# Optimization experiments

Measured on AMD Instinct MI355X. Metric: run time of the kernel, lower is better.

Reference implementation:

```python
import jax, jax.numpy as jnp
import numpy as np

N, B, CIN = 2048, 16, 1
M = 4096
COUT = 64
R = 128


def setup_inputs() -> dict:
    key = jax.random.key(0)
    k1, k2, k3, k4, k5 = jax.random.split(key, 5)
    return {
        "context_in": jax.random.normal(k1, (N, B, CIN), dtype=jnp.float32),
        "context_out": jax.random.normal(k2, (N, B, COUT), dtype=jnp.float32),
        "target_in": jax.random.normal(k3, (M, B, CIN), dtype=jnp.float32),
        "lengthscale": jnp.ones((1,), dtype=jnp.float32),
        "W": jax.random.normal(k4, (R, COUT + 1), dtype=jnp.float32),
        "b": jax.random.normal(k5, (R,), dtype=jnp.float32),
    }


def reference(context_in, context_out, target_in, lengthscale, W, b):
    # context_in: (N,B,Cin), context_out: (N,B,Cout), target_in: (M,B,Cin)
    n, batch, _ = context_in.shape
    # density channel prepended -> (N,B,Cout+1)
    dens = jnp.ones((n, batch, 1), dtype=context_in.dtype)
    co = jnp.concatenate([dens, context_out], axis=-1)
    ci = jnp.transpose(context_in, (1, 0, 2))   # (B,N,Cin)
    ti = jnp.transpose(target_in, (1, 0, 2))    # (B,M,Cin)
    # squared pairwise distances (B,N,M)
    d2 = (jnp.sum(ci * ci, -1)[:, :, None]
          + jnp.sum(ti * ti, -1)[:, None, :]
          - 2.0 * jnp.einsum('bnd,bmd->bnm', ci, ti))
    d2 = jnp.maximum(d2, 0.0)
    # RBF kernel: exp(-0.5 * d2 / lengthscale^2)
    K = jnp.exp(-0.5 * d2 / (lengthscale[0] ** 2))  # (B,N,M)
    # weighted sum over context points: (B,M,Cout+1)
    out = jnp.einsum('nbc,bnm->bmc', co, K)
    # density normalization of non-density channels
    out = jnp.concatenate([out[..., :1], out[..., 1:] / (out[..., :1] + 1e-8)], axis=-1)
    # linear projection (Cout+1 -> R)
    out = out @ W.T + b
    return jnp.transpose(out, (1, 0, 2))  # (M,B,R)
```

## Files before the change

kernel.cpp:

```cpp
#include <hip/hip_runtime.h>
#include <hip/hip_bf16.h>


#define N_CTX 2048
#define BATCH 16
#define M_TGT 4096
#define COUT  64
#define RDIM  128

#define WS_CO_BYTES (N_CTX * BATCH * COUT * 2)
#define WS_SXA_OFF  WS_CO_BYTES
#define WS_SXB_OFF  (WS_SXA_OFF + N_CTX * BATCH * 4)
#define WS_WT_OFF   (WS_SXB_OFF + N_CTX * BATCH * 4)

#define SSCALE 0.8493222f

typedef __attribute__((ext_vector_type(8)))  short        bf16x8;
typedef __attribute__((ext_vector_type(4)))  float        floatx4;
typedef __attribute__((ext_vector_type(4)))  unsigned int uint4v;

#if __has_builtin(__builtin_amdgcn_exp2f)
#define EXP2F __builtin_amdgcn_exp2f
#else
#define EXP2F exp2f
#endif

static __device__ __forceinline__ unsigned int pack_bf16(float lo, float hi) {
    __hip_bfloat162 h = __float22bfloat162_rn(make_float2(lo, hi));
    return *reinterpret_cast<unsigned int*>(&h);
}
static __device__ __forceinline__ unsigned short f2bf(float f) {
    __hip_bfloat16 h = __float2bfloat16(f);
    return *reinterpret_cast<unsigned short*>(&h);
}

__global__ __launch_bounds__(256)
void convdeepset_prep(const float* __restrict__ ci, const float* __restrict__ co,
                      const float* __restrict__ ls, const float* __restrict__ W,
                      unsigned char* __restrict__ ws)
{
    unsigned short* cow = (unsigned short*)ws;
    float*          sxa = (float*)(ws + WS_SXA_OFF);
    float*          sxb = (float*)(ws + WS_SXB_OFF);
    unsigned short* wt  = (unsigned short*)(ws + WS_WT_OFF);
    const int blk = blockIdx.x, tid = threadIdx.x;

    if (blk < 1024) {
        const int g    = blk * 4 + (tid >> 6);
        const int bb   = g & 15;
        const int nblk = g >> 4;
        const int c    = tid & 63;
        const float* rp = co + ((size_t)nblk * 8 * BATCH + bb) * COUT + c;
        unsigned int u[4];
#pragma unroll
        for (int j = 0; j < 4; ++j) {
            const float f0 = rp[(size_t)(2 * j)     * BATCH * COUT];
            const float f1 = rp[(size_t)(2 * j + 1) * BATCH * COUT];
            u[j] = pack_bf16(f0, f1);
        }
        *(uint4v*)&cow[(size_t)bb * 131072 + nblk * 512 + c * 8] = *(uint4v*)u;
    } else if (blk < 1152) {
        const int f = (blk - 1024) * 256 + tid;
        const int n = f & 2047, bb = f >> 11;
        const float s = SSCALE / ls[0];
        const float v = s * ci[(size_t)n * BATCH + bb];
        sxa[bb * 2048 + n] = v + v;
        sxb[bb * 2048 + n] = -v * v;
    } else {
        for (int f = tid; f < 8192; f += 256) {
            const int cp = f & 7, r = (f >> 3) & 127, ch = f >> 10;
            wt[ch * 1024 + r * 8 + cp] = f2bf(W[r * 65 + 1 + ch * 8 + cp]);
        }
    }
}

struct Slot {
    bf16x8  c0, c1, c2, c3;
    floatx4 xa0, xa1, xb0, xb1;
};

__global__ __launch_bounds__(256, 4)
void convdeepset_main(const float* __restrict__ ti, const float* __restrict__ ls,
                      const float* __restrict__ W,  const float* __restrict__ bias,
                      const unsigned char* __restrict__ ws, float* __restrict__ out)
{
    __shared__ float xred[4][64][20];
    __shared__ unsigned short vstage[4][1024];

    const int tid  = threadIdx.x;
    const int lane = tid & 63;
    const int wv   = tid >> 6;
    const int g2   = lane >> 4;
    const int l15  = lane & 15;
    const int wpr  = wv >> 1;
    const int half = wv & 1;

    const int xcd = blockIdx.x & 7;
    const int i   = blockIdx.x >> 3;
    const int b   = xcd * 2 + (i & 1);
    const int mt  = i >> 1;
    const int m0  = mt * 64 + wpr * 32;

    const float s   = SSCALE / ls[0];
    const float sy0 = s * ti[(size_t)(m0 + l15) * BATCH + b];
    const float sy1 = s * ti[(size_t)(m0 + 16 + l15) * BATCH + b];

    const unsigned short* cowb = (const unsigned short*)ws
                               + (size_t)b * 131072 + (size_t)half * 65536;
    const float* sxa = (const float*)(ws + WS_SXA_OFF) + b * N_CTX + half * 1024;
    const float* sxb = (const float*)(ws + WS_SXB_OFF) + b * N_CTX + half * 1024;

    const short onebf = (short)0x3F80;
    bf16x8 ones;
#pragma unroll
    for (int j = 0; j < 8; ++j) ones[j] = onebf;

    floatx4 acc0[4], acc1[4], accd0, accd1;
#pragma unroll
    for (int q = 0; q < 4; ++q)
#pragma unroll
        for (int e = 0; e < 4; ++e) { acc0[q][e] = 0.0f; acc1[q][e] = 0.0f; }
#pragma unroll
    for (int e = 0; e < 4; ++e) { accd0[e] = 0.0f; accd1[e] = 0.0f; }

    auto loadk = [&](Slot& S, int k) {
        const unsigned short* bp = cowb + ((k * 4 + g2) << 9) + l15 * 8;
        S.c0 = *(const bf16x8*)(bp);
        S.c1 = *(const bf16x8*)(bp + 128);
        S.c2 = *(const bf16x8*)(bp + 256);
        S.c3 = *(const bf16x8*)(bp + 384);
        const float* ap  = sxa + k * 32 + g2 * 8;
        const float* bpx = sxb + k * 32 + g2 * 8;
        S.xa0 = *(const floatx4*)(ap);
        S.xa1 = *(const floatx4*)(ap + 4);
        S.xb0 = *(const floatx4*)(bpx);
        S.xb1 = *(const floatx4*)(bpx + 4);
    };

    auto compute = [&](const Slot& S) {
        const floatx4 a00 = S.xa0 * sy0 + S.xb0;
        const floatx4 a01 = S.xa1 * sy0 + S.xb1;
        const floatx4 a10 = S.xa0 * sy1 + S.xb0;
        const floatx4 a11 = S.xa1 * sy1 + S.xb1;
        float kv0[8], kv1[8];
        kv0[0] = EXP2F(a00.x); kv0[1] = EXP2F(a00.y);
        kv0[2] = EXP2F(a00.z); kv0[3] = EXP2F(a00.w);
        kv0[4] = EXP2F(a01.x); kv0[5] = EXP2F(a01.y);
        kv0[6] = EXP2F(a01.z); kv0[7] = EXP2F(a01.w);
        kv1[0] = EXP2F(a10.x); kv1[1] = EXP2F(a10.y);
        kv1[2] = EXP2F(a10.z); kv1[3] = EXP2F(a10.w);
        kv1[4] = EXP2F(a11.x); kv1[5] = EXP2F(a11.y);
        kv1[6] = EXP2F(a11.z); kv1[7] = EXP2F(a11.w);
        uint4v aw0, aw1;
#pragma unroll
        for (int q = 0; q < 4; ++q) {
            aw0[q] = pack_bf16(kv0[2 * q], kv0[2 * q + 1]);
            aw1[q] = pack_bf16(kv1[2 * q], kv1[2 * q + 1]);
        }
        const bf16x8 av0 = __builtin_bit_cast(bf16x8, aw0);
        const bf16x8 av1 = __builtin_bit_cast(bf16x8, aw1);
        acc0[0] = __builtin_amdgcn_mfma_f32_16x16x32_bf16(av0, S.c0, acc0[0], 0, 0, 0);
        acc0[1] = __builtin_amdgcn_mfma_f32_16x16x32_bf16(av0, S.c1, acc0[1], 0, 0, 0);
        acc0[2] = __builtin_amdgcn_mfma_f32_16x16x32_bf16(av0, S.c2, acc0[2], 0, 0, 0);
        acc0[3] = __builtin_amdgcn_mfma_f32_16x16x32_bf16(av0, S.c3, acc0[3], 0, 0, 0);
        accd0   = __builtin_amdgcn_mfma_f32_16x16x32_bf16(av0, ones, accd0, 0, 0, 0);
        acc1[0] = __builtin_amdgcn_mfma_f32_16x16x32_bf16(av1, S.c0, acc1[0], 0, 0, 0);
        acc1[1] = __builtin_amdgcn_mfma_f32_16x16x32_bf16(av1, S.c1, acc1[1], 0, 0, 0);
        acc1[2] = __builtin_amdgcn_mfma_f32_16x16x32_bf16(av1, S.c2, acc1[2], 0, 0, 0);
        acc1[3] = __builtin_amdgcn_mfma_f32_16x16x32_bf16(av1, S.c3, acc1[3], 0, 0, 0);
        accd1   = __builtin_amdgcn_mfma_f32_16x16x32_bf16(av1, ones, accd1, 0, 0, 0);
    };

    Slot A, B;
    loadk(A, 0);
    for (int p = 0; p < 32; p += 2) {
        loadk(B, p + 1);
        compute(A);
        if (p + 2 < 32) loadk(A, p + 2);
        compute(B);
    }

    {
        float* xw = &xred[wv][lane][0];
        const floatx4* wacc = half ? acc0 : acc1;
        const floatx4  wd   = half ? accd0 : accd1;
#pragma unroll
        for (int q = 0; q < 4; ++q) *(floatx4*)&xw[q * 4] = wacc[q];
        *(floatx4*)&xw[16] = wd;
    }
    __syncthreads();
    floatx4  facc[4];
    floatx4  faccd;
    {
        const float* xr = &xred[wv ^ 1][lane][0];
        const floatx4* kacc = half ? acc1 : acc0;
        const floatx4  kd   = half ? accd1 : accd0;
#pragma unroll
        for (int q = 0; q < 4; ++q) facc[q] = kacc[q] + *(const floatx4*)&xr[q * 4];
        faccd = kd + *(const floatx4*)&xr[16];
    }

    const unsigned short* wtg = (const unsigned short*)(ws + WS_WT_OFF);
    const float sysq = half ? sy1 * sy1 : sy0 * sy0;
    const int   mrow = m0 + half * 16;

    float dt[4], ff[4];
#pragma unroll
    for (int reg = 0; reg < 4; ++reg) {
        const int m   = (lane >> 4) * 4 + reg;
        const float ysq = __shfl(sysq, m, 64);
        const float e   = EXP2F(-ysq);
        dt[reg] = faccd[reg] * e;
        ff[reg] = e / (dt[reg] + 1e-8f);
    }
    unsigned short* vs = vstage[wv];
#pragma unroll
    for (int reg = 0; reg < 4; ++reg) {
        const int m = (lane >> 4) * 4 + reg;
#pragma unroll
        for (int q = 0; q < 4; ++q) {
            const int c = q * 16 + l15;
            vs[(c >> 3) * 128 + m * 8 + (c & 7)] = f2bf(facc[q][reg]);
        }
    }
    floatx4 pacc[8];
#pragma unroll
    for (int rt = 0; rt < 8; ++rt)
#pragma unroll
        for (int e = 0; e < 4; ++e) pacc[rt][e] = 0.0f;
#pragma unroll
    for (int s2 = 0; s2 < 2; ++s2) {
        const int ch = s2 * 4 + g2;
        const bf16x8 avp = *(const bf16x8*)&vs[ch * 128 + l15 * 8];
#pragma unroll
        for (int rt = 0; rt < 8; ++rt) {
            const bf16x8 bvp = *(const bf16x8*)&wtg[ch * 1024 + (rt * 16 + l15) * 8];
            pacc[rt] = __builtin_amdgcn_mfma_f32_16x16x32_bf16(avp, bvp, pacc[rt], 0, 0, 0);
        }
    }
#pragma unroll
    for (int rt = 0; rt < 8; ++rt) {
        const int r = rt * 16 + l15;
        const float w0v = W[r * 65];
        const float bv  = bias[r];
#pragma unroll
        for (int reg = 0; reg < 4; ++reg) {
            const int m = (lane >> 4) * 4 + reg;
            out[((size_t)(mrow + m) * BATCH + b) * RDIM + r]
                = pacc[rt][reg] * ff[reg] + dt[reg] * w0v + bv;
        }
    }
}

extern "C" void kernel_launch(void* const* d_in, const int* in_sizes, int n_in,
                              void* d_out, int out_size, void* d_ws, size_t ws_size,
                              hipStream_t stream) {
    const float* ci   = (const float*)d_in[0];
    const float* co   = (const float*)d_in[1];
    const float* ti   = (const float*)d_in[2];
    const float* ls   = (const float*)d_in[3];
    const float* W    = (const float*)d_in[4];
    const float* bias = (const float*)d_in[5];
    float* o = (float*)d_out;
    (void)in_sizes; (void)n_in; (void)out_size; (void)ws_size;

    convdeepset_prep<<<1153, 256, 0, stream>>>(ci, co, ls, W, (unsigned char*)d_ws);
    convdeepset_main<<<1024, 256, 0, stream>>>(
        ti, ls, W, bias, (const unsigned char*)d_ws, o);
}
```

Baseline: 128.5 us.

## Double targets per wave and stage context scalars in LDS

Each wave now covers 64 target rows instead of 32, so each loaded context-output fragment feeds four MFMA row tiles instead of two. This halves the global traffic for context data per output, and the grid shrinks to 512 blocks. The per-batch sxa/sxb arrays are copied into shared memory once per block rather than read from global inside the loop. In exchange, register pressure rises (occupancy bound lowered to 2 blocks per CU), the cross-wave reduction becomes two synchronised rounds, and fewer blocks may leave some CUs underfilled.

```diff
diff --git a/kernel.cpp b/kernel.cpp
--- a/kernel.cpp
+++ b/kernel.cpp
@@ -79,13 +79,15 @@
     floatx4 xa0, xa1, xb0, xb1;
 };
 
-__global__ __launch_bounds__(256, 4)
+__global__ __launch_bounds__(256, 2)
 void convdeepset_main(const float* __restrict__ ti, const float* __restrict__ ls,
                       const float* __restrict__ W,  const float* __restrict__ bias,
                       const unsigned char* __restrict__ ws, float* __restrict__ out)
 {
+    __shared__ float sxal[N_CTX];
+    __shared__ float sxbl[N_CTX];
     __shared__ float xred[4][64][20];
-    __shared__ unsigned short vstage[4][1024];
+    __shared__ unsigned short vstage[4][2][1024];
 
     const int tid  = threadIdx.x;
     const int lane = tid & 63;
@@ -99,29 +101,40 @@
     const int i   = blockIdx.x >> 3;
     const int b   = xcd * 2 + (i & 1);
     const int mt  = i >> 1;
-    const int m0  = mt * 64 + wpr * 32;
-
-    const float s   = SSCALE / ls[0];
-    const float sy0 = s * ti[(size_t)(m0 + l15) * BATCH + b];
-    const float sy1 = s * ti[(size_t)(m0 + 16 + l15) * BATCH + b];
+    const int m0  = mt * 128 + wpr * 64;
+
+    const float4* sag = (const float4*)(ws + WS_SXA_OFF) + b * (N_CTX / 4);
+    const float4* sbg = (const float4*)(ws + WS_SXB_OFF) + b * (N_CTX / 4);
+    ((float4*)sxal)[tid]       = sag[tid];
+    ((float4*)sxal)[tid + 256] = sag[tid + 256];
+    ((float4*)sxbl)[tid]       = sbg[tid];
+    ((float4*)sxbl)[tid + 256] = sbg[tid + 256];
+
+    const float s = SSCALE / ls[0];
+    float syv[4];
+#pragma unroll
+    for (int t = 0; t < 4; ++t)
+        syv[t] = s * ti[(size_t)(m0 + t * 16 + l15) * BATCH + b];
 
     const unsigned short* cowb = (const unsigned short*)ws
                                + (size_t)b * 131072 + (size_t)half * 65536;
-    const float* sxa = (const float*)(ws + WS_SXA_OFF) + b * N_CTX + half * 1024;
-    const float* sxb = (const float*)(ws + WS_SXB_OFF) + b * N_CTX + half * 1024;
+    const int xoff = half * 1024;
 
     const short onebf = (short)0x3F80;
     bf16x8 ones;
 #pragma unroll
     for (int j = 0; j < 8; ++j) ones[j] = onebf;
 
-    floatx4 acc0[4], acc1[4], accd0, accd1;
-#pragma unroll
-    for (int q = 0; q < 4; ++q)
-#pragma unroll
-        for (int e = 0; e < 4; ++e) { acc0[q][e] = 0.0f; acc1[q][e] = 0.0f; }
-#pragma unroll
-    for (int e = 0; e < 4; ++e) { accd0[e] = 0.0f; accd1[e] = 0.0f; }
+    floatx4 acc[4][4], accd[4];
+#pragma unroll
+    for (int t = 0; t < 4; ++t) {
+#pragma unroll
+        for (int q = 0; q < 4; ++q)
+#pragma unroll
+            for (int e = 0; e < 4; ++e) acc[t][q][e] = 0.0f;
+#pragma unroll
+        for (int e = 0; e < 4; ++e) accd[t][e] = 0.0f;
+    }
 
     auto loadk = [&](Slot& S, int k) {
         const unsigned short* bp = cowb + ((k * 4 + g2) << 9) + l15 * 8;
@@ -129,8 +142,8 @@
         S.c1 = *(const bf16x8*)(bp + 128);
         S.c2 = *(const bf16x8*)(bp + 256);
         S.c3 = *(const bf16x8*)(bp + 384);
-        const float* ap  = sxa + k * 32 + g2 * 8;
-        const float* bpx = sxb + k * 32 + g2 * 8;
+        const float* ap  = &sxal[xoff + k * 32 + g2 * 8];
+        const float* bpx = &sxbl[xoff + k * 32 + g2 * 8];
         S.xa0 = *(const floatx4*)(ap);
         S.xa1 = *(const floatx4*)(ap + 4);
         S.xb0 = *(const floatx4*)(bpx);
@@ -138,39 +151,30 @@
     };
 
     auto compute = [&](const Slot& S) {
-        const floatx4 a00 = S.xa0 * sy0 + S.xb0;
-        const floatx4 a01 = S.xa1 * sy0 + S.xb1;
-        const floatx4 a10 = S.xa0 * sy1 + S.xb0;
-        const floatx4 a11 = S.xa1 * sy1 + S.xb1;
-        float kv0[8], kv1[8];
-        kv0[0] = EXP2F(a00.x); kv0[1] = EXP2F(a00.y);
-        kv0[2] = EXP2F(a00.z); kv0[3] = EXP2F(a00.w);
-        kv0[4] = EXP2F(a01.x); kv0[5] = EXP2F(a01.y);
-        kv0[6] = EXP2F(a01.z); kv0[7] = EXP2F(a01.w);
-        kv1[0] = EXP2F(a10.x); kv1[1] = EXP2F(a10.y);
-        kv1[2] = EXP2F(a10.z); kv1[3] = EXP2F(a10.w);
-        kv1[4] = EXP2F(a11.x); kv1[5] = EXP2F(a11.y);
-        kv1[6] = EXP2F(a11.z); kv1[7] = EXP2F(a11.w);
-        uint4v aw0, aw1;
-#pragma unroll
-        for (int q = 0; q < 4; ++q) {
-            aw0[q] = pack_bf16(kv0[2 * q], kv0[2 * q + 1]);
-            aw1[q] = pack_bf16(kv1[2 * q], kv1[2 * q + 1]);
-        }
-        const bf16x8 av0 = __builtin_bit_cast(bf16x8, aw0);
-        const bf16x8 av1 = __builtin_bit_cast(bf16x8, aw1);
-        acc0[0] = __builtin_amdgcn_mfma_f32_16x16x32_bf16(av0, S.c0, acc0[0], 0, 0, 0);
-        acc0[1] = __builtin_amdgcn_mfma_f32_16x16x32_bf16(av0, S.c1, acc0[1], 0, 0, 0);
-        acc0[2] = __builtin_amdgcn_mfma_f32_16x16x32_bf16(av0, S.c2, acc0[2], 0, 0, 0);
-        acc0[3] = __builtin_amdgcn_mfma_f32_16x16x32_bf16(av0, S.c3, acc0[3], 0, 0, 0);
-        accd0   = __builtin_amdgcn_mfma_f32_16x16x32_bf16(av0, ones, accd0, 0, 0, 0);
-        acc1[0] = __builtin_amdgcn_mfma_f32_16x16x32_bf16(av1, S.c0, acc1[0], 0, 0, 0);
-        acc1[1] = __builtin_amdgcn_mfma_f32_16x16x32_bf16(av1, S.c1, acc1[1], 0, 0, 0);
-        acc1[2] = __builtin_amdgcn_mfma_f32_16x16x32_bf16(av1, S.c2, acc1[2], 0, 0, 0);
-        acc1[3] = __builtin_amdgcn_mfma_f32_16x16x32_bf16(av1, S.c3, acc1[3], 0, 0, 0);
-        accd1   = __builtin_amdgcn_mfma_f32_16x16x32_bf16(av1, ones, accd1, 0, 0, 0);
+#pragma unroll
+        for (int t = 0; t < 4; ++t) {
+            const float sy = syv[t];
+            const floatx4 a0 = S.xa0 * sy + S.xb0;
+            const floatx4 a1 = S.xa1 * sy + S.xb1;
+            float kv[8];
+            kv[0] = EXP2F(a0.x); kv[1] = EXP2F(a0.y);
+            kv[2] = EXP2F(a0.z); kv[3] = EXP2F(a0.w);
+            kv[4] = EXP2F(a1.x); kv[5] = EXP2F(a1.y);
+            kv[6] = EXP2F(a1.z); kv[7] = EXP2F(a1.w);
+            uint4v aw;
+#pragma unroll
+            for (int q = 0; q < 4; ++q)
+                aw[q] = pack_bf16(kv[2 * q], kv[2 * q + 1]);
+            const bf16x8 av = __builtin_bit_cast(bf16x8, aw);
+            acc[t][0] = __builtin_amdgcn_mfma_f32_16x16x32_bf16(av, S.c0, acc[t][0], 0, 0, 0);
+            acc[t][1] = __builtin_amdgcn_mfma_f32_16x16x32_bf16(av, S.c1, acc[t][1], 0, 0, 0);
+            acc[t][2] = __builtin_amdgcn_mfma_f32_16x16x32_bf16(av, S.c2, acc[t][2], 0, 0, 0);
+            acc[t][3] = __builtin_amdgcn_mfma_f32_16x16x32_bf16(av, S.c3, acc[t][3], 0, 0, 0);
+            accd[t]   = __builtin_amdgcn_mfma_f32_16x16x32_bf16(av, ones, accd[t], 0, 0, 0);
+        }
     };
 
+    __syncthreads();
     Slot A, B;
     loadk(A, 0);
     for (int p = 0; p < 32; p += 2) {
@@ -180,75 +184,99 @@
         compute(B);
     }
 
-    {
+#pragma unroll
+    for (int j = 0; j < 2; ++j) {
         float* xw = &xred[wv][lane][0];
-        const floatx4* wacc = half ? acc0 : acc1;
-        const floatx4  wd   = half ? accd0 : accd1;
-#pragma unroll
-        for (int q = 0; q < 4; ++q) *(floatx4*)&xw[q * 4] = wacc[q];
-        *(floatx4*)&xw[16] = wd;
-    }
-    __syncthreads();
-    floatx4  facc[4];
-    floatx4  faccd;
-    {
+        if (half == 0) {
+            *(floatx4*)&xw[0]  = acc[2 + j][0];
+            *(floatx4*)&xw[4]  = acc[2 + j][1];
+            *(floatx4*)&xw[8]  = acc[2 + j][2];
+            *(floatx4*)&xw[12] = acc[2 + j][3];
+            *(floatx4*)&xw[16] = accd[2 + j];
+        } else {
+            *(floatx4*)&xw[0]  = acc[j][0];
+            *(floatx4*)&xw[4]  = acc[j][1];
+            *(floatx4*)&xw[8]  = acc[j][2];
+            *(floatx4*)&xw[12] = acc[j][3];
+            *(floatx4*)&xw[16] = accd[j];
+        }
+        __syncthreads();
         const float* xr = &xred[wv ^ 1][lane][0];
-        const floatx4* kacc = half ? acc1 : acc0;
-        const floatx4  kd   = half ? accd1 : accd0;
-#pragma unroll
-        for (int q = 0; q < 4; ++q) facc[q] = kacc[q] + *(const floatx4*)&xr[q * 4];
-        faccd = kd + *(const floatx4*)&xr[16];
+        if (half == 0) {
+            acc[j][0] += *(const floatx4*)&xr[0];
+            acc[j][1] += *(const floatx4*)&xr[4];
+            acc[j][2] += *(const floatx4*)&xr[8];
+            acc[j][3] += *(const floatx4*)&xr[12];
+            accd[j]   += *(const floatx4*)&xr[16];
+        } else {
+            acc[2 + j][0] += *(const floatx4*)&xr[0];
+            acc[2 + j][1] += *(const floatx4*)&xr[4];
+            acc[2 + j][2] += *(const floatx4*)&xr[8];
+            acc[2 + j][3] += *(const floatx4*)&xr[12];
+            accd[2 + j]   += *(const floatx4*)&xr[16];
+        }
+        __syncthreads();
     }
 
     const unsigned short* wtg = (const unsigned short*)(ws + WS_WT_OFF);
-    const float sysq = half ? sy1 * sy1 : sy0 * sy0;
-    const int   mrow = m0 + half * 16;
-
-    float dt[4], ff[4];
-#pragma unroll
-    for (int reg = 0; reg < 4; ++reg) {
-        const int m   = (lane >> 4) * 4 + reg;
-        const float ysq = __shfl(sysq, m, 64);
-        const float e   = EXP2F(-ysq);
-        dt[reg] = faccd[reg] * e;
-        ff[reg] = e / (dt[reg] + 1e-8f);
-    }
-    unsigned short* vs = vstage[wv];
-#pragma unroll
-    for (int reg = 0; reg < 4; ++reg) {
-        const int m = (lane >> 4) * 4 + reg;
-#pragma unroll
-        for (int q = 0; q < 4; ++q) {
-            const int c = q * 16 + l15;
-            vs[(c >> 3) * 128 + m * 8 + (c & 7)] = f2bf(facc[q][reg]);
-        }
-    }
-    floatx4 pacc[8];
-#pragma unroll
-    for (int rt = 0; rt < 8; ++rt)
-#pragma unroll
-        for (int e = 0; e < 4; ++e) pacc[rt][e] = 0.0f;
-#pragma unroll
-    for (int s2 = 0; s2 < 2; ++s2) {
-        const int ch = s2 * 4 + g2;
-        const bf16x8 avp = *(const bf16x8*)&vs[ch * 128 + l15 * 8];
-#pragma unroll
-        for (int rt = 0; rt < 8; ++rt) {
-            const bf16x8 bvp = *(const bf16x8*)&wtg[ch * 1024 + (rt * 16 + l15) * 8];
-            pacc[rt] = __builtin_amdgcn_mfma_f32_16x16x32_bf16(avp, bvp, pacc[rt], 0, 0, 0);
-        }
-    }
-#pragma unroll
-    for (int rt = 0; rt < 8; ++rt) {
-        const int r = rt * 16 + l15;
-        const float w0v = W[r * 65];
-        const float bv  = bias[r];
+
+    auto epi = [&](const floatx4 (&a)[4], const floatx4 ad, float syt, int t, int tt) {
+        const float sysq = syt * syt;
+        const int   mrow = m0 + t * 16;
+        float dt[4], ff[4];
+#pragma unroll
+        for (int reg = 0; reg < 4; ++reg) {
+            const int m   = (lane >> 4) * 4 + reg;
+            const float ysq = __shfl(sysq, m, 64);
+            const float e   = EXP2F(-ysq);
+            dt[reg] = ad[reg] * e;
+            ff[reg] = e / (dt[reg] + 1e-8f);
+        }
+        unsigned short* vs = vstage[wv][tt];
 #pragma unroll
         for (int reg = 0; reg < 4; ++reg) {
             const int m = (lane >> 4) * 4 + reg;
-            out[((size_t)(mrow + m) * BATCH + b) * RDIM + r]
-                = pacc[rt][reg] * ff[reg] + dt[reg] * w0v + bv;
-        }
+#pragma unroll
+            for (int q = 0; q < 4; ++q) {
+                const int c = q * 16 + l15;
+                vs[(c >> 3) * 128 + m * 8 + (c & 7)] = f2bf(a[q][reg]);
+            }
+        }
+        floatx4 pacc[8];
+#pragma unroll
+        for (int rt = 0; rt < 8; ++rt)
+#pragma unroll
+            for (int e = 0; e < 4; ++e) pacc[rt][e] = 0.0f;
+#pragma unroll
+        for (int s2 = 0; s2 < 2; ++s2) {
+            const int ch = s2 * 4 + g2;
+            const bf16x8 avp = *(const bf16x8*)&vs[ch * 128 + l15 * 8];
+#pragma unroll
+            for (int rt = 0; rt < 8; ++rt) {
+                const bf16x8 bvp = *(const bf16x8*)&wtg[ch * 1024 + (rt * 16 + l15) * 8];
+                pacc[rt] = __builtin_amdgcn_mfma_f32_16x16x32_bf16(avp, bvp, pacc[rt], 0, 0, 0);
+            }
+        }
+#pragma unroll
+        for (int rt = 0; rt < 8; ++rt) {
+            const int r = rt * 16 + l15;
+            const float w0v = W[r * 65];
+            const float bv  = bias[r];
+#pragma unroll
+            for (int reg = 0; reg < 4; ++reg) {
+                const int m = (lane >> 4) * 4 + reg;
+                out[((size_t)(mrow + m) * BATCH + b) * RDIM + r]
+                    = pacc[rt][reg] * ff[reg] + dt[reg] * w0v + bv;
+            }
+        }
+    };
+
+    if (half == 0) {
+        epi(acc[0], accd[0], syv[0], 0, 0);
+        epi(acc[1], accd[1], syv[1], 1, 1);
+    } else {
+        epi(acc[2], accd[2], syv[2], 2, 0);
+        epi(acc[3], accd[3], syv[3], 3, 1);
     }
 }
 
@@ -265,6 +293,6 @@
     (void)in_sizes; (void)n_in; (void)out_size; (void)ws_size;
 
     convdeepset_prep<<<1153, 256, 0, stream>>>(ci, co, ls, W, (unsigned char*)d_ws);
-    convdeepset_main<<<1024, 256, 0, stream>>>(
+    convdeepset_main<<<512, 256, 0, stream>>>(
         ti, ls, W, bias, (const unsigned char*)d_ws, o);
 }
```

After: 116.8 us. 9.2% less time.
